# Performance work log

Hardware: AMD Instinct MI355X
Metric: run time of the kernel (lower is better)

The kernel has to match this reference:

```python
import jax, jax.numpy as jnp
import numpy as np

B, N, DIM = 4, 8192, 512
HEADS, DIM_HEAD, M, ITERS = 8, 64, 256, 6
KERNEL = 33


def moore_penrose_pinv(x, iters=ITERS):
    # x: [..., m, m]
    abs_x = jnp.abs(x)
    col = abs_x.sum(axis=-1)
    row = abs_x.sum(axis=-2)
    z = jnp.swapaxes(x, -1, -2) / (jnp.max(col) * jnp.max(row))
    I = jnp.eye(x.shape[-1], dtype=x.dtype)
    for _ in range(iters):
        xz = x @ z
        z = 0.25 * z @ (13.0 * I - xz @ (15.0 * I - xz @ (7.0 * I - xz)))
    return z


def setup_inputs() -> dict:
    key = jax.random.key(0)
    k1, k2, k3, k4 = jax.random.split(key, 4)
    x = jax.random.normal(k1, (B, N, DIM), dtype=jnp.float32)
    w_qkv = jax.random.normal(k2, (DIM, 3 * HEADS * DIM_HEAD), dtype=jnp.float32) * 0.02
    w_out = jax.random.normal(k3, (HEADS * DIM_HEAD, DIM), dtype=jnp.float32) * 0.02
    b_out = jnp.zeros((DIM,), dtype=jnp.float32)
    w_conv = jax.random.normal(k4, (HEADS, 1, KERNEL, 1), dtype=jnp.float32) * 0.02
    return {"x": x, "w_qkv": w_qkv, "w_out": w_out, "b_out": b_out, "w_conv": w_conv}


def reference(x, w_qkv, w_out, b_out, w_conv):
    b, n, _ = x.shape
    h, d, m = HEADS, DIM_HEAD, M
    scale = d ** -0.5
    l = n // m  # n is a multiple of m here (padding path is a no-op)

    qkv = x @ w_qkv  # [b, n, 3*h*d]
    q, k, v = jnp.split(qkv, 3, axis=-1)
    to_heads = lambda t: jnp.transpose(t.reshape(b, n, h, d), (0, 2, 1, 3))  # [b,h,n,d]
    q, k, v = to_heads(q), to_heads(k), to_heads(v)

    q = q * scale
    # landmarks: mean over contiguous blocks of length l
    q_land = q.reshape(b, h, m, l, d).sum(axis=3) / l  # [b,h,m,d]
    k_land = k.reshape(b, h, m, l, d).sum(axis=3) / l

    attn1 = jax.nn.softmax(jnp.einsum('bhid,bhjd->bhij', q, k_land), axis=-1)       # [b,h,n,m]
    attn2 = jax.nn.softmax(jnp.einsum('bhid,bhjd->bhij', q_land, k_land), axis=-1)  # [b,h,m,m]
    attn3 = jax.nn.softmax(jnp.einsum('bhid,bhjd->bhij', q_land, k), axis=-1)       # [b,h,m,n]

    attn2_pinv = moore_penrose_pinv(attn2, ITERS)
    out = attn1 @ (attn2_pinv @ (attn3 @ v))  # [b,h,n,d]

    # depthwise residual conv over the sequence axis (kernel (33,1), groups=heads)
    pad = KERNEL // 2
    res = jax.lax.conv_general_dilated(
        v, w_conv, window_strides=(1, 1), padding=((pad, pad), (0, 0)),
        dimension_numbers=('NCHW', 'OIHW', 'NCHW'), feature_group_count=h)
    out = out + res

    out = jnp.transpose(out, (0, 2, 1, 3)).reshape(b, n, h * d)
    out = out @ w_out + b_out
    return out
```

## Files before the change

### kernel.cpp

```cpp
#include <hip/hip_runtime.h>
#include <cstdint>
#include <cstddef>

#define BQ 4
#define NSEQ 8192
#define DIMC 512
#define NH 8
#define DH 64
#define NM 256
#define NITER 6
#define KW 33
#define BHN (BQ*NH)
#define NSLICE 16
#define JS (NSEQ/NSLICE)

typedef unsigned short bf16u;
typedef __attribute__((ext_vector_type(8))) short short8;
typedef __attribute__((ext_vector_type(4))) float f32x4;
#define MFMA16(a,b,c) __builtin_amdgcn_mfma_f32_16x16x32_bf16(a,b,c,0,0,0)

__device__ inline float b2f(bf16u u) { return __uint_as_float(((unsigned int)u) << 16); }
__device__ inline bf16u f2b(float f) {
  unsigned int u = __float_as_uint(f);
  unsigned int r = (u + 0x7fffu + ((u >> 16) & 1u)) >> 16;
  return (bf16u)r;
}
__device__ inline void splt(float v, unsigned short& h, unsigned short& l) {
  unsigned u = __float_as_uint(v);
  h = (unsigned short)(u >> 16);
  float hf = __uint_as_float(u & 0xffff0000u);
  l = (unsigned short)(__float_as_uint(v - hf) >> 16);
}

__global__ __launch_bounds__(256) void k_fill(float* out, int n, float v) {
  int i = blockIdx.x * 256 + threadIdx.x;
  if (i < n) out[i] = v;
}

__global__ __launch_bounds__(256) void c_prep(
    const float* __restrict__ x, const float* __restrict__ w_qkv, const float* __restrict__ w_out,
    bf16u* __restrict__ xb, bf16u* __restrict__ wqkvT, bf16u* __restrict__ woutT) {
  int id = blockIdx.x;
  if (id < 8192) {
    int i = id*256 + threadIdx.x;
    const float4* s = (const float4*)(x + (size_t)i*8);
    float4 a = s[0], b = s[1];
    ushort4 lo, hi;
    lo.x=f2b(a.x); lo.y=f2b(a.y); lo.z=f2b(a.z); lo.w=f2b(a.w);
    hi.x=f2b(b.x); hi.y=f2b(b.y); hi.z=f2b(b.z); hi.w=f2b(b.w);
    ushort4* d = (ushort4*)(xb + (size_t)i*8);
    d[0] = lo; d[1] = hi;
  } else if (id < 8192+3072) {
    int i = (id-8192)*256 + threadIdx.x;
    int r = i / 1536, c = i - r*1536;
    wqkvT[(size_t)c*DIMC + r] = f2b(w_qkv[i]);
  } else {
    int i = (id-11264)*256 + threadIdx.x;
    int r = i >> 9, c = i & 511;
    woutT[(size_t)c*DIMC + r] = f2b(w_out[i]);
  }
}

template<int MODE>
__global__ __launch_bounds__(256) void k_mgemm(
    const bf16u* __restrict__ A, const bf16u* __restrict__ Bt, int K, int nb,
    bf16u* __restrict__ oq, bf16u* __restrict__ ok, bf16u* __restrict__ ovT,
    const float* __restrict__ bias, float* __restrict__ oC) {
  __shared__ short As[128][72];
  __shared__ short Bs[128][72];
  const int id = blockIdx.x;
  const int rid = (id & 7) * ((int)gridDim.x >> 3) + (id >> 3);
  const int m0 = (rid / nb) * 128, n0 = (rid % nb) * 128;
  const int t = threadIdx.x;
  const int wid = t>>6, l = t&63, lm = l&15, lg = l>>4;
  const int wr = (wid>>1)*64, wc = (wid&1)*64;
  f32x4 acc[4][4];
  #pragma unroll
  for (int i=0;i<4;++i)
    #pragma unroll
    for (int j=0;j<4;++j) acc[i][j] = (f32x4){0,0,0,0};
  for (int k0=0; k0<K; k0+=64) {
    #pragma unroll
    for (int i=0;i<4;++i) {
      int c = t + i*256;
      int row = c>>3, kc = (c&7)<<3;
      *(uint4*)&As[row][kc] = *(const uint4*)(A  + (size_t)(m0+row)*K + k0+kc);
      *(uint4*)&Bs[row][kc] = *(const uint4*)(Bt + (size_t)(n0+row)*K + k0+kc);
    }
    __syncthreads();
    #pragma unroll
    for (int ks=0;ks<2;++ks) {
      short8 af[4], bfr[4];
      #pragma unroll
      for (int i=0;i<4;++i) {
        af[i]  = *(const short8*)&As[wr+i*16+lm][ks*32+lg*8];
        bfr[i] = *(const short8*)&Bs[wc+i*16+lm][ks*32+lg*8];
      }
      #pragma unroll
      for (int i=0;i<4;++i)
        #pragma unroll
        for (int j=0;j<4;++j)
          acc[i][j] = MFMA16(af[i], bfr[j], acc[i][j]);
    }
    __syncthreads();
  }
  if (MODE==0) {
    #pragma unroll
    for (int mt=0;mt<4;++mt) {
      int grb = m0 + wr + mt*16 + lg*4;
      int b_ = grb>>13, nrow = grb & (NSEQ-1);
      #pragma unroll
      for (int nt=0;nt<4;++nt) {
        int gc = n0 + wc + nt*16 + lm;
        int which = gc>>9, h_ = (gc>>6)&7, d = gc&63;
        if (which==2) {
          ushort4 pk;
          pk.x=f2b(acc[mt][nt][0]); pk.y=f2b(acc[mt][nt][1]);
          pk.z=f2b(acc[mt][nt][2]); pk.w=f2b(acc[mt][nt][3]);
          *(ushort4*)(ovT + (((size_t)b_*NH+h_)*DH + d)*NSEQ + nrow) = pk;
        } else {
          bf16u* dst = (which==0) ? oq : ok;
          float mul = (which==0) ? 0.125f : 1.0f;
          #pragma unroll
          for (int r=0;r<4;++r)
            dst[(((size_t)b_*NH+h_)*NSEQ + nrow + r)*DH + d] = f2b(acc[mt][nt][r]*mul);
        }
      }
    }
  } else {
    #pragma unroll
    for (int mt=0;mt<4;++mt)
      #pragma unroll
      for (int r=0;r<4;++r) {
        int gr = m0 + wr + mt*16 + lg*4 + r;
        #pragma unroll
        for (int nt=0;nt<4;++nt) {
          int gc = n0 + wc + nt*16 + lm;
          oC[(size_t)gr*DIMC + gc] = acc[mt][nt][r] + bias[gc];
        }
      }
  }
}

__global__ __launch_bounds__(256) void k_landmarks(
    const bf16u* __restrict__ q, const bf16u* __restrict__ kbuf,
    float* __restrict__ ql, float* __restrict__ klm,
    bf16u* __restrict__ qlb, bf16u* __restrict__ klmb) {
  int gi = blockIdx.x*4 + (threadIdx.x>>6);
  int d = threadIdx.x & 63;
  int bh = gi >> 8, i = gi & 255;
  size_t srcoff = ((size_t)bh*NSEQ + (size_t)i*32)*DH + d;
  float sq = 0, sk = 0;
  #pragma unroll
  for (int j = 0; j < 32; ++j) {
    sq += b2f(q[srcoff + (size_t)j*DH]);
    sk += b2f(kbuf[srcoff + (size_t)j*DH]);
  }
  float mq = sq * (1.0f/32.0f), mk = sk * (1.0f/32.0f);
  ql[(size_t)gi*DH + d]  = mq;  klm[(size_t)gi*DH + d]  = mk;
  qlb[(size_t)gi*DH + d] = f2b(mq); klmb[(size_t)gi*DH + d] = f2b(mk);
}

__global__ __launch_bounds__(256) void k_qlk_exp(
    const float* __restrict__ A, const float* __restrict__ S, float* __restrict__ C, int K) {
  __shared__ short Ah[128][40], Al[128][40], Bh[64][40], Bl[64][40];
  const int bh = blockIdx.y;
  const size_t abase = (size_t)bh*256*K;
  const size_t cbase = (size_t)bh<<16;
  const int m0 = (blockIdx.x & 1)*128, n0 = (blockIdx.x >> 1)*64;
  const int t = threadIdx.x;
  const int wid = t>>6, l = t&63, lm = l&15, lg = l>>4;
  const int wr = (wid&1)*64, wc = (wid>>1)*32;
  f32x4 acc[4][2];
  #pragma unroll
  for (int i=0;i<4;++i) { acc[i][0] = (f32x4){0,0,0,0}; acc[i][1] = (f32x4){0,0,0,0}; }
  for (int k0=0; k0<K; k0+=32) {
    #pragma unroll
    for (int i=0;i<4;++i) {
      int idx = t + i*256;
      int row = idx>>3, kc = (idx&7)<<2;
      float4 v = *(const float4*)(A + abase + (size_t)(m0+row)*K + k0+kc);
      ushort4 hh, ll;
      splt(v.x, hh.x, ll.x); splt(v.y, hh.y, ll.y);
      splt(v.z, hh.z, ll.z); splt(v.w, hh.w, ll.w);
      *(ushort4*)&Ah[row][kc] = hh; *(ushort4*)&Al[row][kc] = ll;
    }
    #pragma unroll
    for (int i=0;i<2;++i) {
      int idx = t + i*256;
      int row = idx>>3, kc = (idx&7)<<2;
      float4 v = *(const float4*)(S + abase + (size_t)(n0+row)*K + k0+kc);
      ushort4 hh, ll;
      splt(v.x, hh.x, ll.x); splt(v.y, hh.y, ll.y);
      splt(v.z, hh.z, ll.z); splt(v.w, hh.w, ll.w);
      *(ushort4*)&Bh[row][kc] = hh; *(ushort4*)&Bl[row][kc] = ll;
    }
    __syncthreads();
    short8 ah[4], al[4], sh[2], sl[2];
    #pragma unroll
    for (int mt=0;mt<4;++mt) {
      ah[mt] = *(const short8*)&Ah[wr+mt*16+lm][lg*8];
      al[mt] = *(const short8*)&Al[wr+mt*16+lm][lg*8];
    }
    #pragma unroll
    for (int nt=0;nt<2;++nt) {
      sh[nt] = *(const short8*)&Bh[wc+nt*16+lm][lg*8];
      sl[nt] = *(const short8*)&Bl[wc+nt*16+lm][lg*8];
    }
    #pragma unroll
    for (int mt=0;mt<4;++mt)
      #pragma unroll
      for (int nt=0;nt<2;++nt) {
        acc[mt][nt] = MFMA16(ah[mt], sh[nt], acc[mt][nt]);
        acc[mt][nt] = MFMA16(ah[mt], sl[nt], acc[mt][nt]);
        acc[mt][nt] = MFMA16(al[mt], sh[nt], acc[mt][nt]);
      }
    __syncthreads();
  }
  #pragma unroll
  for (int mt=0;mt<4;++mt)
    #pragma unroll
    for (int nt=0;nt<2;++nt)
      #pragma unroll
      for (int r=0;r<4;++r) {
        int gr = m0 + wr + mt*16 + lg*4 + r;
        int gc = n0 + wc + nt*16 + lm;
        C[cbase + (size_t)gr*256 + gc] = __expf(acc[mt][nt][r]);
      }
}

__global__ __launch_bounds__(256) void k_rowsm(float* __restrict__ a2, unsigned* __restrict__ scal) {
  if (blockIdx.x == 0 && threadIdx.x < 2) scal[threadIdx.x] = 0u;
  int row = blockIdx.x*4 + (threadIdx.x>>6);
  int l = threadIdx.x & 63;
  float4* p = (float4*)(a2 + (size_t)row*256 + l*4);
  float4 v = *p;
  float s = v.x+v.y+v.z+v.w;
  #pragma unroll
  for (int d=1; d<64; d<<=1) s += __shfl_xor(s, d);
  float inv = 1.0f/s;
  v.x*=inv; v.y*=inv; v.z*=inv; v.w*=inv;
  *p = v;
}

__global__ __launch_bounds__(256) void k_pinv_reduce(const float* __restrict__ a2, unsigned* scal) {
  int bh = blockIdx.x, t = threadIdx.x;
  const float* A = a2 + (size_t)bh*NM*NM;
  float rs = 0, cs = 0;
  for (int j = 0; j < NM; ++j) rs += fabsf(A[(size_t)t*NM + j]);
  for (int i = 0; i < NM; ++i) cs += fabsf(A[(size_t)i*NM + t]);
  __shared__ float red[256];
  red[t] = rs; __syncthreads();
  for (int s = 128; s > 0; s >>= 1) { if (t < s) red[t] = fmaxf(red[t], red[t+s]); __syncthreads(); }
  if (t == 0) atomicMax(scal+0, __float_as_uint(red[0]));
  __syncthreads();
  red[t] = cs; __syncthreads();
  for (int s = 128; s > 0; s >>= 1) { if (t < s) red[t] = fmaxf(red[t], red[t+s]); __syncthreads(); }
  if (t == 0) atomicMax(scal+1, __float_as_uint(red[0]));
}

__global__ __launch_bounds__(256) void k_split_init(
    const float* __restrict__ a2, const unsigned* __restrict__ scal,
    bf16u* __restrict__ a2h, bf16u* __restrict__ a2l,
    bf16u* __restrict__ zch, bf16u* __restrict__ zcl) {
  __shared__ bf16u Th[64][72], Tl[64][72];
  const int bh = blockIdx.y;
  const int tx = blockIdx.x & 3, ty = blockIdx.x >> 2;
  const int r0 = ty*64, c0 = tx*64;
  const size_t base = (size_t)bh<<16;
  const int t = threadIdx.x;
  const float rc = 1.0f/(__uint_as_float(scal[0]) * __uint_as_float(scal[1]));
  {
    int rr = t>>2, cc0 = (t&3)*16;
    const float* src = a2 + base + (size_t)(r0+rr)*256 + c0+cc0;
    bf16u hbuf[16], lbuf[16];
    #pragma unroll
    for (int u=0;u<4;++u) {
      float4 v = *(const float4*)(src + u*4);
      float vv[4] = {v.x,v.y,v.z,v.w};
      #pragma unroll
      for (int e=0;e<4;++e) {
        splt(vv[e], hbuf[u*4+e], lbuf[u*4+e]);
        bf16u zh_, zl_;
        splt(vv[e]*rc, zh_, zl_);
        Th[cc0+u*4+e][rr] = zh_;
        Tl[cc0+u*4+e][rr] = zl_;
      }
    }
    bf16u* dh = a2h + base + (size_t)(r0+rr)*256 + c0+cc0;
    bf16u* dl = a2l + base + (size_t)(r0+rr)*256 + c0+cc0;
    #pragma unroll
    for (int u=0;u<4;++u) {
      *(ushort4*)(dh + u*4) = *(ushort4*)&hbuf[u*4];
      *(ushort4*)(dl + u*4) = *(ushort4*)&lbuf[u*4];
    }
  }
  __syncthreads();
  {
    int cc = t>>2, rr0 = (t&3)*16;
    bf16u* dh = zch + base + (size_t)(c0+cc)*256 + r0+rr0;
    bf16u* dl = zcl + base + (size_t)(c0+cc)*256 + r0+rr0;
    #pragma unroll
    for (int u=0;u<4;++u) {
      *(ushort4*)(dh + u*4) = *(ushort4*)&Th[cc][rr0+u*4];
      *(ushort4*)(dl + u*4) = *(ushort4*)&Tl[cc][rr0+u*4];
    }
  }
}

template<int PHASE>
__global__ __launch_bounds__(256) void k_ns(
    const bf16u* __restrict__ Ah, const bf16u* __restrict__ Al,
    const bf16u* __restrict__ A2h, const bf16u* __restrict__ A2l,
    const bf16u* __restrict__ Bh_, const bf16u* __restrict__ Bl_,
    const bf16u* __restrict__ Xh, const bf16u* __restrict__ Xl,
    const bf16u* __restrict__ X2h, const bf16u* __restrict__ X2l,
    bf16u* __restrict__ Oh, bf16u* __restrict__ Ol,
    bf16u* __restrict__ O2h, bf16u* __restrict__ O2l,
    bf16u* __restrict__ Ch, bf16u* __restrict__ Cl,
    const unsigned* __restrict__ scal) {
  __shared__ short AhS[128][36], AlS[128][36], BhS[64][36], BlS[64][36];
  const int z = (gridDim.z == 2) ? blockIdx.z : (PHASE==2 ? 1 : 0);
  const int bh = blockIdx.y;
  const size_t base = (size_t)bh<<16;
  const int m0 = (blockIdx.x & 1)*128, n0 = (blockIdx.x >> 1)*64;
  const int t = threadIdx.x;
  const int wid = t>>6, l = t&63, lm = l&15, lg = l>>4;
  const int wr = (wid&1)*64, wc = (wid>>1)*32;
  const bf16u* pAh = z ? A2h : Ah;
  const bf16u* pAl = z ? A2l : Al;
  f32x4 acc[4][2];
  #pragma unroll
  for (int i=0;i<4;++i) { acc[i][0] = (f32x4){0,0,0,0}; acc[i][1] = (f32x4){0,0,0,0}; }
  for (int k0=0; k0<256; k0+=32) {
    #pragma unroll
    for (int i=0;i<2;++i) {
      int idx = t + i*256;
      int row = idx>>2, ch = (idx&3)<<3;
      *(uint4*)&AhS[row][ch] = *(const uint4*)(pAh + base + (size_t)(m0+row)*256 + k0+ch);
      *(uint4*)&AlS[row][ch] = *(const uint4*)(pAl + base + (size_t)(m0+row)*256 + k0+ch);
    }
    {
      int row = t>>2, ch = (t&3)<<3;
      *(uint4*)&BhS[row][ch] = *(const uint4*)(Bh_ + base + (size_t)(n0+row)*256 + k0+ch);
      *(uint4*)&BlS[row][ch] = *(const uint4*)(Bl_ + base + (size_t)(n0+row)*256 + k0+ch);
    }
    __syncthreads();
    short8 ah[4], al[4], sh[2], sl[2];
    #pragma unroll
    for (int mt=0;mt<4;++mt) {
      ah[mt] = *(const short8*)&AhS[wr+mt*16+lm][lg*8];
      al[mt] = *(const short8*)&AlS[wr+mt*16+lm][lg*8];
    }
    #pragma unroll
    for (int nt=0;nt<2;++nt) {
      sh[nt] = *(const short8*)&BhS[wc+nt*16+lm][lg*8];
      sl[nt] = *(const short8*)&BlS[wc+nt*16+lm][lg*8];
    }
    #pragma unroll
    for (int mt=0;mt<4;++mt)
      #pragma unroll
      for (int nt=0;nt<2;++nt) {
        acc[mt][nt] = MFMA16(ah[mt], sh[nt], acc[mt][nt]);
        acc[mt][nt] = MFMA16(ah[mt], sl[nt], acc[mt][nt]);
        acc[mt][nt] = MFMA16(al[mt], sh[nt], acc[mt][nt]);
      }
    __syncthreads();
  }
  float rc = 1.0f;
  if (PHASE==0) rc = 1.0f/(__uint_as_float(scal[0]) * __uint_as_float(scal[1]));
  #pragma unroll
  for (int mt=0;mt<4;++mt)
    #pragma unroll
    for (int nt=0;nt<2;++nt)
      #pragma unroll
      for (int r=0;r<4;++r) {
        int gr = m0 + wr + mt*16 + lg*4 + r;
        int gc = n0 + wc + nt*16 + lm;
        size_t idx = base + (size_t)gr*256 + gc;
        float a = acc[mt][nt][r];
        bf16u hh, ll;
        if (PHASE==0) {
          splt(a*rc, hh, ll); Oh[idx]=hh; Ol[idx]=ll;
        } else if (PHASE==1) {
          if (z==0) {
            splt(a, hh, ll); Oh[idx]=hh; Ol[idx]=ll;
            float wv = b2f(Xh[idx]) + b2f(Xl[idx]);
            float cb = ((gr==gc)?15.0f:0.0f) - 7.0f*wv + a;
            splt(cb, hh, ll); Ch[idx]=hh; Cl[idx]=ll;
          } else {
            splt(a, hh, ll); O2h[idx]=hh; O2l[idx]=ll;
          }
        } else {
          if (z==0) {
            float xv = b2f(Xh[idx]) + b2f(Xl[idx]);
            splt(3.25f*xv - 0.25f*a, hh, ll); Oh[idx]=hh; Ol[idx]=ll;
          } else {
            float xv = b2f(X2h[idx]) + b2f(X2l[idx]);
            splt(3.25f*xv - 0.25f*a, hh, ll); O2h[idx]=hh; O2l[idx]=ll;
          }
        }
      }
}

template<int MODE>
__global__ __launch_bounds__(256) void k_flash(
    const bf16u* __restrict__ qg, const bf16u* __restrict__ kg,
    const bf16u* __restrict__ vtg, float* __restrict__ fpart, bf16u* __restrict__ outb) {
  constexpr int NCH = (MODE==0) ? (JS/64) : 4;
  const int bh = blockIdx.y;
  const int tile = blockIdx.x;
  const int t = threadIdx.x;
  const int wid = t>>6, l = t&63, lm = l&15, lg = l>>4;
  const size_t NQbase = (MODE==0) ? ((size_t)bh*NM) : ((size_t)bh*NSEQ + (size_t)tile*256);
  const int NJ = (MODE==0) ? NSEQ : NM;
  const int j0base = (MODE==0) ? tile*JS : 0;

  __shared__ short Ks[64][72];
  __shared__ short Vs[64][72];
  __shared__ short Pt[4][64][72];

  short8 qf[4][2];
  {
    const bf16u* qrow = qg + (NQbase + (size_t)wid*64) * DH;
    #pragma unroll
    for (int mt=0;mt<4;++mt)
      #pragma unroll
      for (int ks=0;ks<2;++ks)
        qf[mt][ks] = *(const short8*)(qrow + (size_t)(mt*16+lm)*DH + ks*32 + lg*8);
  }
  f32x4 oacc[4][4];
  #pragma unroll
  for (int i=0;i<4;++i)
    #pragma unroll
    for (int j=0;j<4;++j) oacc[i][j] = (f32x4){0,0,0,0};
  float rs[4][4];
  #pragma unroll
  for (int i=0;i<4;++i) { rs[i][0]=0; rs[i][1]=0; rs[i][2]=0; rs[i][3]=0; }

  const bf16u* kbh = kg  + (size_t)bh*NJ*DH;
  const bf16u* vbh = vtg + (size_t)bh*DH*NJ;

  for (int ch=0; ch<NCH; ++ch) {
    int j0 = j0base + ch*64;
    #pragma unroll
    for (int i=0;i<2;++i) {
      int c = t + i*256;
      int row = c>>3, kc = (c&7)<<3;
      *(uint4*)&Ks[row][kc] = *(const uint4*)(kbh + (size_t)(j0+row)*DH + kc);
      *(uint4*)&Vs[row][kc] = *(const uint4*)(vbh + (size_t)row*NJ + j0 + kc);
    }
    __syncthreads();
    short8 kf[4][2];
    #pragma unroll
    for (int jt=0;jt<4;++jt)
      #pragma unroll
      for (int ks=0;ks<2;++ks)
        kf[jt][ks] = *(const short8*)&Ks[jt*16+lm][ks*32+lg*8];
    #pragma unroll
    for (int mt=0;mt<4;++mt) {
      #pragma unroll
      for (int jt=0;jt<4;++jt) {
        f32x4 s = (f32x4){0,0,0,0};
        s = MFMA16(qf[mt][0], kf[jt][0], s);
        s = MFMA16(qf[mt][1], kf[jt][1], s);
        #pragma unroll
        for (int r=0;r<4;++r) {
          float p = __expf(s[r]);
          rs[mt][r] += p;
          Pt[wid][mt*16+lg*4+r][jt*16+lm] = f2b(p);
        }
      }
    }
    short8 vf[4][2];
    #pragma unroll
    for (int dt=0;dt<4;++dt)
      #pragma unroll
      for (int jw=0;jw<2;++jw)
        vf[dt][jw] = *(const short8*)&Vs[dt*16+lm][jw*32+lg*8];
    #pragma unroll
    for (int mt=0;mt<4;++mt) {
      short8 pa0 = *(const short8*)&Pt[wid][mt*16+lm][lg*8];
      short8 pa1 = *(const short8*)&Pt[wid][mt*16+lm][32+lg*8];
      #pragma unroll
      for (int dt=0;dt<4;++dt) {
        oacc[mt][dt] = MFMA16(pa0, vf[dt][0], oacc[mt][dt]);
        oacc[mt][dt] = MFMA16(pa1, vf[dt][1], oacc[mt][dt]);
      }
    }
    __syncthreads();
  }
  #pragma unroll
  for (int mt=0;mt<4;++mt)
    #pragma unroll
    for (int r=0;r<4;++r) {
      float v = rs[mt][r];
      v += __shfl_xor(v, 1); v += __shfl_xor(v, 2);
      v += __shfl_xor(v, 4); v += __shfl_xor(v, 8);
      rs[mt][r] = v;
    }
  if (MODE==0) {
    float* fb = fpart + (((size_t)bh*NSLICE + tile)*NM)*65;
    #pragma unroll
    for (int mt=0;mt<4;++mt)
      #pragma unroll
      for (int r=0;r<4;++r) {
        int row = wid*64 + mt*16 + lg*4 + r;
        float* fr = fb + (size_t)row*65;
        #pragma unroll
        for (int dt=0;dt<4;++dt) fr[dt*16+lm] = oacc[mt][dt][r];
        if (lm==0) fr[64] = rs[mt][r];
      }
  } else {
    const int b_ = bh>>3, h_ = bh&7;
    #pragma unroll
    for (int mt=0;mt<4;++mt)
      #pragma unroll
      for (int r=0;r<4;++r) {
        float inv = 1.0f/rs[mt][r];
        int n = tile*256 + wid*64 + mt*16 + lg*4 + r;
        bf16u* orow = outb + ((size_t)b_*NSEQ + n)*DIMC + h_*DH;
        #pragma unroll
        for (int dt=0;dt<4;++dt)
          orow[dt*16+lm] = f2b(oacc[mt][dt][r]*inv);
      }
  }
}

__global__ __launch_bounds__(256) void k_attn3v_combine(
    const float* __restrict__ fpart, float* __restrict__ w1T) {
  int gi = blockIdx.x*4 + (threadIdx.x>>6);
  int d = threadIdx.x & 63;
  int bh = gi >> 8, i = gi & 255;
  float accd = 0, ssum = 0;
  #pragma unroll
  for (int s = 0; s < NSLICE; ++s) {
    const float* fp = fpart + (((size_t)bh*NSLICE + s)*NM + i)*65;
    accd += fp[d];
    ssum += fp[64];
  }
  w1T[((size_t)bh*64 + d)*256 + i] = accd / ssum;
}

__global__ __launch_bounds__(256) void k_w2nat(
    const float* __restrict__ w1T, const bf16u* __restrict__ zh, const bf16u* __restrict__ zl,
    bf16u* __restrict__ w2T) {
  __shared__ short Ah[64][36], Al[64][36], Bh[64][36], Bl[64][36];
  const int bh = blockIdx.y;
  const int n0 = blockIdx.x*64;
  const size_t a0 = (size_t)bh*64*256;
  const size_t s0 = (size_t)bh<<16;
  const int t = threadIdx.x;
  const int wid = t>>6, l = t&63, lm = l&15, lg = l>>4;
  const int wc = wid*16;
  f32x4 acc[4];
  #pragma unroll
  for (int i=0;i<4;++i) acc[i] = (f32x4){0,0,0,0};
  for (int k0=0; k0<256; k0+=32) {
    #pragma unroll
    for (int i=0;i<2;++i) {
      int idx = t + i*256;
      int row = idx>>3, kc = (idx&7)<<2;
      float4 v = *(const float4*)(w1T + a0 + (size_t)row*256 + k0+kc);
      ushort4 hh, ll;
      splt(v.x, hh.x, ll.x); splt(v.y, hh.y, ll.y);
      splt(v.z, hh.z, ll.z); splt(v.w, hh.w, ll.w);
      *(ushort4*)&Ah[row][kc] = hh; *(ushort4*)&Al[row][kc] = ll;
    }
    {
      int row = t>>2, ch = (t&3)<<3;
      *(uint4*)&Bh[row][ch] = *(const uint4*)(zh + s0 + (size_t)(n0+row)*256 + k0+ch);
      *(uint4*)&Bl[row][ch] = *(const uint4*)(zl + s0 + (size_t)(n0+row)*256 + k0+ch);
    }
    __syncthreads();
    short8 sh = *(const short8*)&Bh[wc+lm][lg*8];
    short8 sl = *(const short8*)&Bl[wc+lm][lg*8];
    #pragma unroll
    for (int mt=0;mt<4;++mt) {
      short8 ah = *(const short8*)&Ah[mt*16+lm][lg*8];
      short8 al = *(const short8*)&Al[mt*16+lm][lg*8];
      acc[mt] = MFMA16(ah, sh, acc[mt]);
      acc[mt] = MFMA16(ah, sl, acc[mt]);
      acc[mt] = MFMA16(al, sh, acc[mt]);
    }
    __syncthreads();
  }
  #pragma unroll
  for (int mt=0;mt<4;++mt)
    #pragma unroll
    for (int r=0;r<4;++r) {
      int gm = mt*16 + lg*4 + r;
      w2T[a0 + (size_t)gm*256 + n0 + wc + lm] = f2b(acc[mt][r]);
    }
}

__global__ __launch_bounds__(256) void k_conv_add(
    const bf16u* __restrict__ vt, const float* __restrict__ wc, bf16u* __restrict__ outb) {
  __shared__ short Vs[288][72];
  __shared__ float Wsh[40];
  const int bh = blockIdx.y, n0 = blockIdx.x*256;
  const int b_ = bh>>3, h_ = bh&7;
  const int t = threadIdx.x;
  if (t < KW) Wsh[t] = wc[h_*KW + t];
  const bf16u* vrow = vt + (size_t)bh*DH*NSEQ;
  {
    int d = t&63, seg = t>>6;
    #pragma unroll
    for (int u=0; u<9; ++u) {
      int nl = seg*72 + u*8;
      int gn = n0 - 16 + nl;
      bf16u e8[8];
      if (gn >= 0 && gn + 8 <= NSEQ) {
        *(uint4*)e8 = *(const uint4*)(vrow + (size_t)d*NSEQ + gn);
      } else {
        #pragma unroll
        for (int e=0;e<8;++e) {
          int g = gn + e;
          e8[e] = (g>=0 && g<NSEQ) ? vrow[(size_t)d*NSEQ + g] : (bf16u)0;
        }
      }
      #pragma unroll
      for (int e=0;e<8;++e) Vs[nl+e][d] = e8[e];
    }
  }
  __syncthreads();
  const int d = t&63, q = t>>6;
  #pragma unroll
  for (int c2=0;c2<4;++c2) {
    int nb = q*64 + c2*16;
    float wv[48];
    #pragma unroll
    for (int i=0;i<48;++i) wv[i] = b2f(Vs[nb+i][d]);
    #pragma unroll
    for (int e=0;e<16;++e) {
      float s = 0;
      #pragma unroll
      for (int k=0;k<KW;++k) s = fmaf(wv[e+k], Wsh[k], s);
      size_t oi = ((size_t)b_*NSEQ + n0 + nb + e)*DIMC + h_*DH + d;
      outb[oi] = f2b(b2f(outb[oi]) + s);
    }
  }
}

extern "C" void kernel_launch(void* const* d_in, const int* in_sizes, int n_in,
                              void* d_out, int out_size, void* d_ws, size_t ws_size,
                              hipStream_t stream) {
  (void)in_sizes; (void)n_in;
  const float* x      = (const float*)d_in[0];
  const float* w_qkv  = (const float*)d_in[1];
  const float* w_out  = (const float*)d_in[2];
  const float* b_out  = (const float*)d_in[3];
  const float* w_conv = (const float*)d_in[4];
  float* out = (float*)d_out;

  const size_t QKV_E = (size_t)BHN*NSEQ*DH;
  const size_t LM_E  = (size_t)BHN*NM*DH;
  const size_t MM_E  = (size_t)BHN*NM*NM;
  const size_t PLSZ  = MM_E*2;

  char* p = (char*)d_ws;
  char* nsb   = p;          p += 9*PLSZ;
  bf16u* zch  = (bf16u*)p;  p += PLSZ;
  bf16u* zcl  = (bf16u*)p;  p += PLSZ;
  bf16u* qb    = (bf16u*)p; p += QKV_E*2;
  bf16u* kb    = (bf16u*)p; p += QKV_E*2;
  bf16u* vT    = (bf16u*)p; p += QKV_E*2;
  bf16u* wqkvT = (bf16u*)p; p += (size_t)DIMC*3*DIMC*2;
  bf16u* woutT = (bf16u*)p; p += (size_t)DIMC*DIMC*2;
  float* ql    = (float*)p; p += LM_E*4;
  float* klm   = (float*)p; p += LM_E*4;
  bf16u* qlb   = (bf16u*)p; p += LM_E*2;
  bf16u* klmb  = (bf16u*)p; p += LM_E*2;
  float* w1T   = (float*)p; p += LM_E*4;
  bf16u* w2T   = (bf16u*)p; p += LM_E*2;
  unsigned* scal = (unsigned*)p; p += 256;
  size_t need = (size_t)(p - (char*)d_ws);

  if (ws_size < need) {
    k_fill<<<(out_size + 255)/256, 256, 0, stream>>>(out, out_size, 12345.0f);
    return;
  }

  bf16u* a2h  = (bf16u*)(nsb + 0*PLSZ);
  bf16u* a2l  = (bf16u*)(nsb + 1*PLSZ);
  bf16u* s1h  = (bf16u*)(nsb + 2*PLSZ);
  bf16u* s1l  = (bf16u*)(nsb + 3*PLSZ);
  bf16u* cmh  = (bf16u*)(nsb + 4*PLSZ);
  bf16u* cml  = (bf16u*)(nsb + 5*PLSZ);
  bf16u* wh   = (bf16u*)(nsb + 6*PLSZ);
  bf16u* wl   = (bf16u*)(nsb + 7*PLSZ);
  float* a2f  = (float*)(nsb + 2*PLSZ);
  float* fpart = (float*)nsb;
  bf16u* c1h = a2h; bf16u* c1l = a2l;
  bf16u* xb  = (bf16u*)nsb;

  c_prep<<<12288, 256, 0, stream>>>(x, w_qkv, w_out, xb, wqkvT, woutT);
  k_mgemm<0><<<3072, 256, 0, stream>>>(xb, wqkvT, DIMC, 12, qb, kb, vT, nullptr, nullptr);
  k_landmarks<<<(BHN*NM)/4, 256, 0, stream>>>(qb, kb, ql, klm, qlb, klmb);
  k_qlk_exp<<<dim3(8, BHN), 256, 0, stream>>>(ql, klm, a2f, DH);
  k_rowsm<<<BHN*NM/4, 256, 0, stream>>>(a2f, scal);
  k_pinv_reduce<<<BHN, 256, 0, stream>>>(a2f, scal);
  k_split_init<<<dim3(16, BHN), 256, 0, stream>>>(a2f, scal, a2h, a2l, zch, zcl);
  k_ns<0><<<dim3(8, BHN, 1), 256, 0, stream>>>(
      a2h,a2l, nullptr,nullptr, a2h,a2l, nullptr,nullptr, nullptr,nullptr,
      wh,wl, nullptr,nullptr, nullptr,nullptr, scal);
  for (int it = 0; it < NITER; ++it) {
    k_ns<1><<<dim3(8, BHN, 2), 256, 0, stream>>>(
        wh,wl, zch,zcl, wh,wl, wh,wl, nullptr,nullptr,
        s1h,s1l, c1h,c1l, cmh,cml, nullptr);
    k_ns<2><<<dim3(8, BHN, (it==NITER-1)?1:2), 256, 0, stream>>>(
        s1h,s1l, c1h,c1l, cmh,cml, wh,wl, zch,zcl,
        wh,wl, zch,zcl, nullptr,nullptr, nullptr);
  }
  k_flash<0><<<dim3(NSLICE, BHN), 256, 0, stream>>>(qlb, kb, vT, fpart, nullptr);
  k_attn3v_combine<<<(BHN*NM)/4, 256, 0, stream>>>(fpart, w1T);
  k_w2nat<<<dim3(4, BHN), 256, 0, stream>>>(w1T, zch, zcl, w2T);
  bf16u* outb = kb;
  k_flash<1><<<dim3(NSEQ/256, BHN), 256, 0, stream>>>(qb, klmb, w2T, nullptr, outb);
  k_conv_add<<<dim3(NSEQ/256, BHN), 256, 0, stream>>>(vT, w_conv, outb);
  k_mgemm<1><<<1024, 256, 0, stream>>>(outb, woutT, DIMC, 4, nullptr, nullptr, nullptr, b_out, out);
}
```

Baseline: 688.2 us.

## Double-buffer LDS tiles with register prefetch in projection and Newton-Schulz GEMMs

Both the QKV/output projection GEMM and the Newton-Schulz pinv GEMM now keep two LDS buffers. Each step loads the next K-slice into registers while MFMAs run on the current buffer, then stores it to the other buffer, leaving one barrier per step instead of two. The projection GEMM's K-step shrinks from 64 to 32, which halves the work done between barriers. The aim is to hide global-load latency behind compute, at the cost of more registers, which may lower occupancy.

```diff
diff --git a/kernel.cpp b/kernel.cpp
--- a/kernel.cpp
+++ b/kernel.cpp
@@ -66,44 +66,72 @@
     const bf16u* __restrict__ A, const bf16u* __restrict__ Bt, int K, int nb,
     bf16u* __restrict__ oq, bf16u* __restrict__ ok, bf16u* __restrict__ ovT,
     const float* __restrict__ bias, float* __restrict__ oC) {
-  __shared__ short As[128][72];
-  __shared__ short Bs[128][72];
+  __shared__ short As[2][128][36];
+  __shared__ short Bs[2][128][36];
   const int id = blockIdx.x;
   const int rid = (id & 7) * ((int)gridDim.x >> 3) + (id >> 3);
   const int m0 = (rid / nb) * 128, n0 = (rid % nb) * 128;
   const int t = threadIdx.x;
   const int wid = t>>6, l = t&63, lm = l&15, lg = l>>4;
   const int wr = (wid>>1)*64, wc = (wid&1)*64;
+  const int srow = t>>2, skc = (t&3)<<3;
   f32x4 acc[4][4];
   #pragma unroll
   for (int i=0;i<4;++i)
     #pragma unroll
     for (int j=0;j<4;++j) acc[i][j] = (f32x4){0,0,0,0};
-  for (int k0=0; k0<K; k0+=64) {
+  uint4 ra[2], rb[2];
+  #pragma unroll
+  for (int i=0;i<2;++i) {
+    int idx = t + i*256;
+    int row = idx>>2, kc = (idx&3)<<3;
+    ra[i] = *(const uint4*)(A  + (size_t)(m0+row)*K + kc);
+    rb[i] = *(const uint4*)(Bt + (size_t)(n0+row)*K + kc);
+  }
+  #pragma unroll
+  for (int i=0;i<2;++i) {
+    int idx = t + i*256;
+    int row = idx>>2, kc = (idx&3)<<3;
+    *(uint4*)&As[0][row][kc] = ra[i];
+    *(uint4*)&Bs[0][row][kc] = rb[i];
+  }
+  __syncthreads();
+  const int nsteps = K >> 5;
+  for (int s = 0; s < nsteps; ++s) {
+    const int cur = s & 1;
+    if (s+1 < nsteps) {
+      int k0 = (s+1) << 5;
+      #pragma unroll
+      for (int i=0;i<2;++i) {
+        int idx = t + i*256;
+        int row = idx>>2, kc = (idx&3)<<3;
+        ra[i] = *(const uint4*)(A  + (size_t)(m0+row)*K + k0+kc);
+        rb[i] = *(const uint4*)(Bt + (size_t)(n0+row)*K + k0+kc);
+      }
+    }
+    short8 af[4], bfr[4];
     #pragma unroll
     for (int i=0;i<4;++i) {
-      int c = t + i*256;
-      int row = c>>3, kc = (c&7)<<3;
-      *(uint4*)&As[row][kc] = *(const uint4*)(A  + (size_t)(m0+row)*K + k0+kc);
-      *(uint4*)&Bs[row][kc] = *(const uint4*)(Bt + (size_t)(n0+row)*K + k0+kc);
-    }
-    __syncthreads();
-    #pragma unroll
-    for (int ks=0;ks<2;++ks) {
-      short8 af[4], bfr[4];
-      #pragma unroll
-      for (int i=0;i<4;++i) {
-        af[i]  = *(const short8*)&As[wr+i*16+lm][ks*32+lg*8];
-        bfr[i] = *(const short8*)&Bs[wc+i*16+lm][ks*32+lg*8];
-      }
-      #pragma unroll
-      for (int i=0;i<4;++i)
-        #pragma unroll
-        for (int j=0;j<4;++j)
-          acc[i][j] = MFMA16(af[i], bfr[j], acc[i][j]);
-    }
-    __syncthreads();
-  }
+      af[i]  = *(const short8*)&As[cur][wr+i*16+lm][lg*8];
+      bfr[i] = *(const short8*)&Bs[cur][wc+i*16+lm][lg*8];
+    }
+    #pragma unroll
+    for (int i=0;i<4;++i)
+      #pragma unroll
+      for (int j=0;j<4;++j)
+        acc[i][j] = MFMA16(af[i], bfr[j], acc[i][j]);
+    if (s+1 < nsteps) {
+      #pragma unroll
+      for (int i=0;i<2;++i) {
+        int idx = t + i*256;
+        int row = idx>>2, kc = (idx&3)<<3;
+        *(uint4*)&As[cur^1][row][kc] = ra[i];
+        *(uint4*)&Bs[cur^1][row][kc] = rb[i];
+      }
+      __syncthreads();
+    }
+  }
+  (void)srow; (void)skc;
   if (MODE==0) {
     #pragma unroll
     for (int mt=0;mt<4;++mt) {
@@ -319,7 +347,7 @@
     bf16u* __restrict__ O2h, bf16u* __restrict__ O2l,
     bf16u* __restrict__ Ch, bf16u* __restrict__ Cl,
     const unsigned* __restrict__ scal) {
-  __shared__ short AhS[128][36], AlS[128][36], BhS[64][36], BlS[64][36];
+  __shared__ short AhS[2][128][36], AlS[2][128][36], BhS[2][64][36], BlS[2][64][36];
   const int z = (gridDim.z == 2) ? blockIdx.z : (PHASE==2 ? 1 : 0);
   const int bh = blockIdx.y;
   const size_t base = (size_t)bh<<16;
@@ -332,30 +360,55 @@
   f32x4 acc[4][2];
   #pragma unroll
   for (int i=0;i<4;++i) { acc[i][0] = (f32x4){0,0,0,0}; acc[i][1] = (f32x4){0,0,0,0}; }
-  for (int k0=0; k0<256; k0+=32) {
-    #pragma unroll
-    for (int i=0;i<2;++i) {
-      int idx = t + i*256;
-      int row = idx>>2, ch = (idx&3)<<3;
-      *(uint4*)&AhS[row][ch] = *(const uint4*)(pAh + base + (size_t)(m0+row)*256 + k0+ch);
-      *(uint4*)&AlS[row][ch] = *(const uint4*)(pAl + base + (size_t)(m0+row)*256 + k0+ch);
-    }
-    {
-      int row = t>>2, ch = (t&3)<<3;
-      *(uint4*)&BhS[row][ch] = *(const uint4*)(Bh_ + base + (size_t)(n0+row)*256 + k0+ch);
-      *(uint4*)&BlS[row][ch] = *(const uint4*)(Bl_ + base + (size_t)(n0+row)*256 + k0+ch);
-    }
-    __syncthreads();
+  uint4 rah[2], ral[2], rbh, rbl;
+  const int arow = t>>2, akc = (t&3)<<3;
+  const int brow = t>>2, bkc = (t&3)<<3;
+  #pragma unroll
+  for (int i=0;i<2;++i) {
+    int idx = t + i*256;
+    int row = idx>>2, kc = (idx&3)<<3;
+    rah[i] = *(const uint4*)(pAh + base + (size_t)(m0+row)*256 + kc);
+    ral[i] = *(const uint4*)(pAl + base + (size_t)(m0+row)*256 + kc);
+  }
+  {
+    int row = brow & 63, kc = bkc;
+    rbh = *(const uint4*)(Bh_ + base + (size_t)(n0+row)*256 + kc);
+    rbl = *(const uint4*)(Bl_ + base + (size_t)(n0+row)*256 + kc);
+  }
+  #pragma unroll
+  for (int i=0;i<2;++i) {
+    int idx = t + i*256;
+    int row = idx>>2, kc = (idx&3)<<3;
+    *(uint4*)&AhS[0][row][kc] = rah[i];
+    *(uint4*)&AlS[0][row][kc] = ral[i];
+  }
+  *(uint4*)&BhS[0][brow & 63][bkc] = rbh;
+  *(uint4*)&BlS[0][brow & 63][bkc] = rbl;
+  __syncthreads();
+  for (int s = 0; s < 8; ++s) {
+    const int cur = s & 1;
+    if (s < 7) {
+      int k0 = (s+1) << 5;
+      #pragma unroll
+      for (int i=0;i<2;++i) {
+        int idx = t + i*256;
+        int row = idx>>2, kc = (idx&3)<<3;
+        rah[i] = *(const uint4*)(pAh + base + (size_t)(m0+row)*256 + k0+kc);
+        ral[i] = *(const uint4*)(pAl + base + (size_t)(m0+row)*256 + k0+kc);
+      }
+      rbh = *(const uint4*)(Bh_ + base + (size_t)(n0+(brow&63))*256 + k0+bkc);
+      rbl = *(const uint4*)(Bl_ + base + (size_t)(n0+(brow&63))*256 + k0+bkc);
+    }
     short8 ah[4], al[4], sh[2], sl[2];
     #pragma unroll
     for (int mt=0;mt<4;++mt) {
-      ah[mt] = *(const short8*)&AhS[wr+mt*16+lm][lg*8];
-      al[mt] = *(const short8*)&AlS[wr+mt*16+lm][lg*8];
+      ah[mt] = *(const short8*)&AhS[cur][wr+mt*16+lm][lg*8];
+      al[mt] = *(const short8*)&AlS[cur][wr+mt*16+lm][lg*8];
     }
     #pragma unroll
     for (int nt=0;nt<2;++nt) {
-      sh[nt] = *(const short8*)&BhS[wc+nt*16+lm][lg*8];
-      sl[nt] = *(const short8*)&BlS[wc+nt*16+lm][lg*8];
+      sh[nt] = *(const short8*)&BhS[cur][wc+nt*16+lm][lg*8];
+      sl[nt] = *(const short8*)&BlS[cur][wc+nt*16+lm][lg*8];
     }
     #pragma unroll
     for (int mt=0;mt<4;++mt)
@@ -365,8 +418,20 @@
         acc[mt][nt] = MFMA16(ah[mt], sl[nt], acc[mt][nt]);
         acc[mt][nt] = MFMA16(al[mt], sh[nt], acc[mt][nt]);
       }
-    __syncthreads();
-  }
+    if (s < 7) {
+      #pragma unroll
+      for (int i=0;i<2;++i) {
+        int idx = t + i*256;
+        int row = idx>>2, kc = (idx&3)<<3;
+        *(uint4*)&AhS[cur^1][row][kc] = rah[i];
+        *(uint4*)&AlS[cur^1][row][kc] = ral[i];
+      }
+      *(uint4*)&BhS[cur^1][brow & 63][bkc] = rbh;
+      *(uint4*)&BlS[cur^1][brow & 63][bkc] = rbl;
+      __syncthreads();
+    }
+  }
+  (void)arow; (void)akc;
   float rc = 1.0f;
   if (PHASE==0) rc = 1.0f/(__uint_as_float(scal[0]) * __uint_as_float(scal[1]));
   #pragma unroll
```

New measurement: 902.9 us. +31.2%, slower.
